# Performance work log

Hardware: AMD Instinct MI355X
Metric: run time of the kernel (lower is better)

Reference implementation:

```python
import jax, jax.numpy as jnp
import numpy as np

N = 100000      # nodes
E = 1600000     # edges (avg degree 16)
DIN = 128
DOUT = 128


def setup_inputs() -> dict:
    key = jax.random.key(0)
    k1, k2, k3, k4 = jax.random.split(key, 4)
    x = jax.random.normal(k1, (N, DIN), dtype=jnp.float32)
    edge_index = jax.random.randint(k2, (2, E), 0, N, dtype=jnp.int64)
    # guarantee every node appears at least once as a source row so that
    # degree > 0 everywhere (1/sqrt(0) would be inf, as in the torch code)
    row = edge_index[0].at[:N].set(jnp.arange(N, dtype=jnp.int64))
    edge_index = jnp.stack([row, edge_index[1]])
    W = jax.random.normal(k3, (DOUT, DIN), dtype=jnp.float32) / np.sqrt(DIN)
    b = jax.random.normal(k4, (DOUT,), dtype=jnp.float32) * 0.01
    return {"x": x, "edge_index": edge_index, "W": W, "b": b}


def reference(x, edge_index, W, b):
    # Math identical to: A = dense(add_self_loops(edge_index));
    # D = 1/sqrt(degree(edge_index[0]))  (degree WITHOUT self-loops);
    # out = (D_i * A_ij * D_j) @ (x W^T + b)
    row, col = edge_index[0], edge_index[1]
    deg = jax.ops.segment_sum(jnp.ones(row.shape[0], x.dtype), row, num_segments=N)
    d = jax.lax.rsqrt(deg)                      # [N]
    h = x @ W.T + b                             # [N, DOUT]
    # edge contributions: out[r] += D[r] * D[c] * h[c]  (duplicate edges sum, as to_dense does)
    agg = jax.ops.segment_sum(d[col][:, None] * h[col], row, num_segments=N)
    # self-loop term added for every node: D[i]^2 * h[i]
    out = d[:, None] * agg + (d * d)[:, None] * h
    return out
```

## Files before the change

### kernel.cpp

```cpp
#include <hip/hip_runtime.h>

#define D 128
#define BROWS 512
#define LOGB 9
#define NBMAX 256
#define CAP 9216
#define CHUNK 4096

typedef __attribute__((ext_vector_type(8))) short bf16x8;
typedef __attribute__((ext_vector_type(4))) float f32x4;

__device__ inline unsigned short f2bf(float f) {
    unsigned u = __float_as_uint(f);
    u += 0x7FFFu + ((u >> 16) & 1u);
    return (unsigned short)(u >> 16);
}
__device__ inline float bf2f(unsigned short h) {
    return __uint_as_float((unsigned)h << 16);
}
__device__ inline float bflo(unsigned u) { return __uint_as_float(u << 16); }
__device__ inline float bfhi(unsigned u) { return __uint_as_float(u & 0xFFFF0000u); }

__global__ __launch_bounds__(512) void k_bin(const int* __restrict__ row,
                                             const int* __restrict__ col,
                                             int E, int* __restrict__ gcur,
                                             unsigned* __restrict__ ebuf,
                                             const float* __restrict__ W,
                                             unsigned short* __restrict__ Wbh,
                                             unsigned short* __restrict__ Wbl) {
    __shared__ int lhist[NBMAX];
    __shared__ int sc[NBMAX];
    __shared__ int gbase[NBMAX];
    __shared__ unsigned sstage[CHUNK];
    __shared__ int sdest[CHUNK];
    int t = threadIdx.x;
    if (blockIdx.x < 8) {
        int base = blockIdx.x * 2048 + t;
        #pragma unroll
        for (int i = 0; i < 4; ++i) {
            int idx = base + i * 512;
            float wv = W[idx];
            unsigned short h = f2bf(wv);
            Wbh[idx] = h;
            Wbl[idx] = f2bf(wv - bf2f(h));
        }
    }
    int base = blockIdx.x * CHUNK;
    if (t < NBMAX) lhist[t] = 0;
    __syncthreads();
    int b[8], p[8]; unsigned pk[8];
    #pragma unroll
    for (int i = 0; i < 8; ++i) {
        int idx = base + i * 512 + t;
        if (idx < E) {
            int r = row[idx], c = col[idx];
            b[i] = r >> LOGB;
            pk[i] = ((unsigned)(r & (BROWS - 1)) << 17) | (unsigned)c;
            p[i] = atomicAdd(&lhist[b[i]], 1);
        } else b[i] = -1;
    }
    __syncthreads();
    if (t < 64) {
        int a0 = lhist[4*t], a1 = lhist[4*t+1], a2 = lhist[4*t+2], a3 = lhist[4*t+3];
        int s = a0 + a1 + a2 + a3;
        int incl = s;
        #pragma unroll
        for (int m = 1; m < 64; m <<= 1) {
            int tmp = __shfl_up(incl, m);
            if (t >= m) incl += tmp;
        }
        int excl = incl - s;
        sc[4*t] = excl; sc[4*t+1] = excl + a0;
        sc[4*t+2] = excl + a0 + a1; sc[4*t+3] = excl + a0 + a1 + a2;
        if (a0 > 0) gbase[4*t]   = atomicAdd(&gcur[4*t],   a0);
        if (a1 > 0) gbase[4*t+1] = atomicAdd(&gcur[4*t+1], a1);
        if (a2 > 0) gbase[4*t+2] = atomicAdd(&gcur[4*t+2], a2);
        if (a3 > 0) gbase[4*t+3] = atomicAdd(&gcur[4*t+3], a3);
    }
    __syncthreads();
    #pragma unroll
    for (int i = 0; i < 8; ++i) {
        if (b[i] >= 0) {
            int lidx = sc[b[i]] + p[i];
            int rel = gbase[b[i]] + p[i];
            sstage[lidx] = pk[i];
            sdest[lidx] = (rel < CAP) ? (b[i] * CAP + rel) : -1;
        }
    }
    __syncthreads();
    int total = sc[NBMAX - 1] + lhist[NBMAX - 1];
    for (int i = t; i < total; i += 512) {
        int d = sdest[i];
        if (d >= 0) ebuf[d] = sstage[i];
    }
}

__global__ __launch_bounds__(1024) void k_group(const int* __restrict__ gcur,
                                                const unsigned* __restrict__ ebuf,
                                                const float* __restrict__ x,
                                                int N, int NBK,
                                                float* __restrict__ dvals,
                                                int* __restrict__ rptr,
                                                int* __restrict__ csr_col,
                                                unsigned short* __restrict__ xs) {
    __shared__ unsigned sebuf[CAP];
    __shared__ int lhist[BROWS];
    __shared__ float sdl[BROWS];
    __shared__ int wtot[8];
    __shared__ int woff[8];
    __shared__ int sebase;
    int bkt = blockIdx.x, t = threadIdx.x;
    int cnt = gcur[bkt]; if (cnt > CAP) cnt = CAP;
    if (t < 64) {
        int acc = 0;
        for (int i = t; i < bkt; i += 64) {
            int g = gcur[i];
            acc += (g > CAP) ? CAP : g;
        }
        #pragma unroll
        for (int m = 1; m < 64; m <<= 1) acc += __shfl_xor(acc, m);
        if (t == 0) sebase = acc;
    }
    if (t < BROWS) lhist[t] = 0;
    __syncthreads();
    const unsigned* ep = ebuf + (size_t)bkt * CAP;
    for (int i = t; i < cnt; i += 1024) {
        unsigned e = ep[i];
        sebuf[i] = e;
        atomicAdd(&lhist[e >> 17], 1);
    }
    __syncthreads();
    int lane = t & 63, wv = t >> 6;
    int v = 0, incl = 0;
    if (t < BROWS) {
        v = lhist[t];
        incl = v;
        #pragma unroll
        for (int m = 1; m < 64; m <<= 1) {
            int tmp = __shfl_up(incl, m);
            if (lane >= m) incl += tmp;
        }
        if (lane == 63) wtot[wv] = incl;
    }
    __syncthreads();
    if (t < 8) {
        int w = wtot[t];
        int wincl = w;
        #pragma unroll
        for (int m = 1; m < 8; m <<= 1) {
            int tmp = __shfl_up(wincl, m);
            if (t >= m) wincl += tmp;
        }
        woff[t] = wincl - w;
    }
    __syncthreads();
    int ebase = sebase;
    if (t < BROWS) {
        int excl = woff[wv] + incl - v;
        int r = (bkt << LOGB) + t;
        float dl = rsqrtf((float)v);
        if (r < N) {
            rptr[r] = ebase + excl;
            dvals[r] = dl;
        }
        sdl[t] = dl;
        lhist[t] = excl;
    }
    if (bkt == NBK - 1 && t == 0) rptr[N] = ebase + cnt;
    if (bkt == 0 && t == 0) dvals[N] = 0.f;
    __syncthreads();
    for (int i = t; i < cnt; i += 1024) {
        unsigned e = sebuf[i];
        int rr = (int)(e >> 17);
        int p = atomicAdd(&lhist[rr], 1);
        csr_col[ebase + p] = (int)(e & 0x1FFFFu);
    }
    int rb = bkt << LOGB;
    const float4* x4 = (const float4*)x;
    for (int idx = t; idx < BROWS * 32; idx += 1024) {
        int rl = idx >> 5;
        int r = rb + rl;
        if (r < N) {
            float4 vv = x4[(size_t)r * 32 + (idx & 31)];
            float d = sdl[rl];
            ushort4 o = make_ushort4(f2bf(d * vv.x), f2bf(d * vv.y),
                                     f2bf(d * vv.z), f2bf(d * vv.w));
            ((ushort4*)xs)[(size_t)r * 32 + (idx & 31)] = o;
        }
    }
    if (bkt == 0 && t < 64)
        ((unsigned*)(xs + (size_t)N * D))[t] = 0u;
}

#define ACC8(v) do { \
    a[0] += bflo((v).x); a[1] += bfhi((v).x); \
    a[2] += bflo((v).y); a[3] += bfhi((v).y); \
    a[4] += bflo((v).z); a[5] += bfhi((v).z); \
    a[6] += bflo((v).w); a[7] += bfhi((v).w); } while (0)

__global__ __launch_bounds__(256) void k_rows(const unsigned short* __restrict__ xs,
                                              const int* __restrict__ rptr,
                                              const int* __restrict__ csr_col,
                                              const float* __restrict__ dvals,
                                              float* __restrict__ ssum,
                                              float* __restrict__ y, int N) {
    int wid = (blockIdx.x * blockDim.x + threadIdx.x) >> 6;
    if (wid >= N) return;
    int lane = threadIdx.x & 63;
    int grp = lane >> 4, sl = lane & 15;
    int s = rptr[wid];
    int n = rptr[wid + 1] - s;
    const uint4* xsv = (const uint4*)xs;

    int cc = csr_col[s + lane];
    int ccreg = (lane < n) ? cc : N;
    float sd = dvals[ccreg];
    uint4 vself = xsv[(size_t)wid * 16 + sl];

    float a[8] = {0.f, 0.f, 0.f, 0.f, 0.f, 0.f, 0.f, 0.f};
    int nf = (n < 64) ? n : 64;
    for (int k0 = 0; k0 < nf; k0 += 16) {
        int i0 = k0 + grp;
        int c0 = __shfl(ccreg, i0);
        int c1 = __shfl(ccreg, i0 + 4);
        int c2 = __shfl(ccreg, i0 + 8);
        int c3 = __shfl(ccreg, i0 + 12);
        uint4 v0 = xsv[(size_t)c0 * 16 + sl];
        uint4 v1 = xsv[(size_t)c1 * 16 + sl];
        uint4 v2 = xsv[(size_t)c2 * 16 + sl];
        uint4 v3 = xsv[(size_t)c3 * 16 + sl];
        __builtin_amdgcn_sched_group_barrier(0x020, 4, 0);
        ACC8(v0); ACC8(v1); ACC8(v2); ACC8(v3);
        __builtin_amdgcn_sched_group_barrier(0x002, 64, 0);
    }
    if (__builtin_expect(n > 64, 0)) {
        for (int idx = 64 + grp; idx < n; idx += 4) {
            int c = csr_col[s + idx];
            uint4 v = xsv[(size_t)c * 16 + sl];
            ACC8(v);
        }
        for (int idx = 64 + lane; idx < n; idx += 64)
            sd += dvals[csr_col[s + idx]];
    }
    if (grp == 0) ACC8(vself);

    #pragma unroll
    for (int j = 0; j < 8; ++j) {
        a[j] += __shfl_xor(a[j], 16);
        a[j] += __shfl_xor(a[j], 32);
    }
    #pragma unroll
    for (int m = 1; m < 64; m <<= 1) sd += __shfl_xor(sd, m);

    float dr = dvals[wid];
    if (grp < 2) {
        float4 o = (grp == 0) ? make_float4(a[0], a[1], a[2], a[3])
                              : make_float4(a[4], a[5], a[6], a[7]);
        o.x *= dr; o.y *= dr; o.z *= dr; o.w *= dr;
        ((float4*)(y + (size_t)wid * D))[sl * 2 + grp] = o;
    }
    if (lane == 0) ssum[wid] = dr * (dr + sd);
}

#define LDSW 136

__global__ __launch_bounds__(256, 2) void k_gemm(const unsigned short* __restrict__ Wbh,
                                                 const unsigned short* __restrict__ Wbl,
                                                 const float* __restrict__ b,
                                                 const float* __restrict__ ssum,
                                                 float* yo, int N) {
    __shared__ unsigned short Whi[128 * LDSW];
    __shared__ unsigned short Wlo[128 * LDSW];
    __shared__ float bs[D];
    int t = threadIdx.x;
    #pragma unroll
    for (int i = 0; i < 16; ++i) {
        int idx4 = i * 256 + t;
        int r = idx4 >> 5;
        int c = (idx4 & 31) * 4;
        ((ushort4*)&Whi[r * LDSW + c])[0] = ((const ushort4*)Wbh)[idx4];
        ((ushort4*)&Wlo[r * LDSW + c])[0] = ((const ushort4*)Wbl)[idx4];
    }
    if (t < D) bs[t] = b[t];
    __syncthreads();

    int wave = t >> 6, lane = t & 63;
    int quad = lane >> 4, mrow = lane & 15;
    int row_base = blockIdx.x * 128 + wave * 32;

    bf16x8 Ahi[2][4], Alo[2][4];
    #pragma unroll
    for (int s = 0; s < 2; ++s) {
        int grow = row_base + s * 16 + mrow;
        bool ok = grow < N;
        const float* yrow = yo + (size_t)(ok ? grow : 0) * D;
        #pragma unroll
        for (int kk = 0; kk < 4; ++kk) {
            int k0 = kk * 32 + quad * 8;
            float4 f0 = ok ? ((const float4*)(yrow + k0))[0] : make_float4(0, 0, 0, 0);
            float4 f1 = ok ? ((const float4*)(yrow + k0))[1] : make_float4(0, 0, 0, 0);
            float fv[8] = {f0.x, f0.y, f0.z, f0.w, f1.x, f1.y, f1.z, f1.w};
            #pragma unroll
            for (int j = 0; j < 8; ++j) {
                unsigned short h = f2bf(fv[j]);
                Ahi[s][kk][j] = (short)h;
                Alo[s][kk][j] = (short)f2bf(fv[j] - bf2f(h));
            }
        }
    }

    f32x4 acc[2][8];
    #pragma unroll
    for (int s = 0; s < 2; ++s)
        #pragma unroll
        for (int ct = 0; ct < 8; ++ct)
            acc[s][ct] = (f32x4){0.f, 0.f, 0.f, 0.f};

    #pragma unroll
    for (int ct = 0; ct < 8; ++ct) {
        int wrow = ct * 16 + mrow;
        #pragma unroll
        for (int kk = 0; kk < 4; ++kk) {
            int off = wrow * LDSW + kk * 32 + quad * 8;
            bf16x8 Bhi = *(const bf16x8*)&Whi[off];
            bf16x8 Blo = *(const bf16x8*)&Wlo[off];
            #pragma unroll
            for (int s = 0; s < 2; ++s) {
                acc[s][ct] = __builtin_amdgcn_mfma_f32_16x16x32_bf16(Ahi[s][kk], Bhi, acc[s][ct], 0, 0, 0);
                acc[s][ct] = __builtin_amdgcn_mfma_f32_16x16x32_bf16(Alo[s][kk], Bhi, acc[s][ct], 0, 0, 0);
                acc[s][ct] = __builtin_amdgcn_mfma_f32_16x16x32_bf16(Ahi[s][kk], Blo, acc[s][ct], 0, 0, 0);
            }
        }
    }

    #pragma unroll
    for (int s = 0; s < 2; ++s) {
        #pragma unroll
        for (int r = 0; r < 4; ++r) {
            int grow = row_base + s * 16 + quad * 4 + r;
            if (grow < N) {
                float sv = ssum[grow];
                #pragma unroll
                for (int ct = 0; ct < 8; ++ct) {
                    int col = ct * 16 + mrow;
                    yo[(size_t)grow * D + col] = acc[s][ct][r] + sv * bs[col];
                }
            }
        }
    }
}

extern "C" void kernel_launch(void* const* d_in, const int* in_sizes, int n_in,
                              void* d_out, int out_size, void* d_ws, size_t ws_size,
                              hipStream_t stream) {
    const float* x  = (const float*)d_in[0];
    const int*   ei = (const int*)d_in[1];
    const float* W  = (const float*)d_in[2];
    const float* b  = (const float*)d_in[3];
    float* out = (float*)d_out;
    int N = in_sizes[0] / D;
    int E = in_sizes[1] / 2;
    int NB = (N + BROWS - 1) / BROWS;
    int NCH = (E + CHUNK - 1) / CHUNK;

    int*            gcur    = (int*)d_ws;
    int*            rptr    = gcur + NBMAX;
    float*          dvals   = (float*)(rptr + N + 1);
    float*          ssum    = dvals + N + 1;
    int*            csr_col = (int*)(ssum + N);
    unsigned*       ebuf    = (unsigned*)(csr_col + E + 64);
    unsigned short* Wbh     = (unsigned short*)(ebuf + (size_t)NB * CAP);
    unsigned short* Wbl     = Wbh + D * D;
    uintptr_t xs_addr = (uintptr_t)(Wbl + D * D);
    xs_addr = (xs_addr + 15) & ~(uintptr_t)15;
    unsigned short* xs = (unsigned short*)xs_addr;

    hipMemsetAsync(gcur, 0, NBMAX * sizeof(int), stream);
    k_bin<<<NCH, 512, 0, stream>>>(ei, ei + E, E, gcur, ebuf, W, Wbh, Wbl);
    k_group<<<NB, 1024, 0, stream>>>(gcur, ebuf, x, N, NB, dvals, rptr, csr_col, xs);
    k_rows<<<(N + 3) / 4, 256, 0, stream>>>(xs, rptr, csr_col, dvals, ssum, out, N);
    k_gemm<<<(N + 127) / 128, 256, 0, stream>>>(Wbh, Wbl, b, ssum, out, N);
}
```

Baseline: 275.3 us.

## Reorder pipeline: transform first, then aggregate pre-scaled bf16 H

```diff
diff --git a/kernel.cpp b/kernel.cpp
--- a/kernel.cpp
+++ b/kernel.cpp
@@ -6,6 +6,7 @@
 #define NBMAX 256
 #define CAP 9216
 #define CHUNK 4096
+#define LDSW 136
 
 typedef __attribute__((ext_vector_type(8))) short bf16x8;
 typedef __attribute__((ext_vector_type(4))) float f32x4;
@@ -97,15 +98,13 @@
 
 __global__ __launch_bounds__(1024) void k_group(const int* __restrict__ gcur,
                                                 const unsigned* __restrict__ ebuf,
-                                                const float* __restrict__ x,
                                                 int N, int NBK,
                                                 float* __restrict__ dvals,
                                                 int* __restrict__ rptr,
                                                 int* __restrict__ csr_col,
-                                                unsigned short* __restrict__ xs) {
+                                                unsigned short* __restrict__ Hs) {
     __shared__ unsigned sebuf[CAP];
     __shared__ int lhist[BROWS];
-    __shared__ float sdl[BROWS];
     __shared__ int wtot[8];
     __shared__ int woff[8];
     __shared__ int sebase;
@@ -158,16 +157,16 @@
     if (t < BROWS) {
         int excl = woff[wv] + incl - v;
         int r = (bkt << LOGB) + t;
-        float dl = rsqrtf((float)v);
         if (r < N) {
             rptr[r] = ebase + excl;
-            dvals[r] = dl;
-        }
-        sdl[t] = dl;
+            dvals[r] = rsqrtf((float)v);
+        }
         lhist[t] = excl;
     }
     if (bkt == NBK - 1 && t == 0) rptr[N] = ebase + cnt;
     if (bkt == 0 && t == 0) dvals[N] = 0.f;
+    if (bkt == 0 && t < 64)
+        ((unsigned*)(Hs + (size_t)N * D))[t] = 0u;
     __syncthreads();
     for (int i = t; i < cnt; i += 1024) {
         unsigned e = sebuf[i];
@@ -175,100 +174,14 @@
         int p = atomicAdd(&lhist[rr], 1);
         csr_col[ebase + p] = (int)(e & 0x1FFFFu);
     }
-    int rb = bkt << LOGB;
-    const float4* x4 = (const float4*)x;
-    for (int idx = t; idx < BROWS * 32; idx += 1024) {
-        int rl = idx >> 5;
-        int r = rb + rl;
-        if (r < N) {
-            float4 vv = x4[(size_t)r * 32 + (idx & 31)];
-            float d = sdl[rl];
-            ushort4 o = make_ushort4(f2bf(d * vv.x), f2bf(d * vv.y),
-                                     f2bf(d * vv.z), f2bf(d * vv.w));
-            ((ushort4*)xs)[(size_t)r * 32 + (idx & 31)] = o;
-        }
-    }
-    if (bkt == 0 && t < 64)
-        ((unsigned*)(xs + (size_t)N * D))[t] = 0u;
-}
-
-#define ACC8(v) do { \
-    a[0] += bflo((v).x); a[1] += bfhi((v).x); \
-    a[2] += bflo((v).y); a[3] += bfhi((v).y); \
-    a[4] += bflo((v).z); a[5] += bfhi((v).z); \
-    a[6] += bflo((v).w); a[7] += bfhi((v).w); } while (0)
-
-__global__ __launch_bounds__(256) void k_rows(const unsigned short* __restrict__ xs,
-                                              const int* __restrict__ rptr,
-                                              const int* __restrict__ csr_col,
-                                              const float* __restrict__ dvals,
-                                              float* __restrict__ ssum,
-                                              float* __restrict__ y, int N) {
-    int wid = (blockIdx.x * blockDim.x + threadIdx.x) >> 6;
-    if (wid >= N) return;
-    int lane = threadIdx.x & 63;
-    int grp = lane >> 4, sl = lane & 15;
-    int s = rptr[wid];
-    int n = rptr[wid + 1] - s;
-    const uint4* xsv = (const uint4*)xs;
-
-    int cc = csr_col[s + lane];
-    int ccreg = (lane < n) ? cc : N;
-    float sd = dvals[ccreg];
-    uint4 vself = xsv[(size_t)wid * 16 + sl];
-
-    float a[8] = {0.f, 0.f, 0.f, 0.f, 0.f, 0.f, 0.f, 0.f};
-    int nf = (n < 64) ? n : 64;
-    for (int k0 = 0; k0 < nf; k0 += 16) {
-        int i0 = k0 + grp;
-        int c0 = __shfl(ccreg, i0);
-        int c1 = __shfl(ccreg, i0 + 4);
-        int c2 = __shfl(ccreg, i0 + 8);
-        int c3 = __shfl(ccreg, i0 + 12);
-        uint4 v0 = xsv[(size_t)c0 * 16 + sl];
-        uint4 v1 = xsv[(size_t)c1 * 16 + sl];
-        uint4 v2 = xsv[(size_t)c2 * 16 + sl];
-        uint4 v3 = xsv[(size_t)c3 * 16 + sl];
-        __builtin_amdgcn_sched_group_barrier(0x020, 4, 0);
-        ACC8(v0); ACC8(v1); ACC8(v2); ACC8(v3);
-        __builtin_amdgcn_sched_group_barrier(0x002, 64, 0);
-    }
-    if (__builtin_expect(n > 64, 0)) {
-        for (int idx = 64 + grp; idx < n; idx += 4) {
-            int c = csr_col[s + idx];
-            uint4 v = xsv[(size_t)c * 16 + sl];
-            ACC8(v);
-        }
-        for (int idx = 64 + lane; idx < n; idx += 64)
-            sd += dvals[csr_col[s + idx]];
-    }
-    if (grp == 0) ACC8(vself);
-
-    #pragma unroll
-    for (int j = 0; j < 8; ++j) {
-        a[j] += __shfl_xor(a[j], 16);
-        a[j] += __shfl_xor(a[j], 32);
-    }
-    #pragma unroll
-    for (int m = 1; m < 64; m <<= 1) sd += __shfl_xor(sd, m);
-
-    float dr = dvals[wid];
-    if (grp < 2) {
-        float4 o = (grp == 0) ? make_float4(a[0], a[1], a[2], a[3])
-                              : make_float4(a[4], a[5], a[6], a[7]);
-        o.x *= dr; o.y *= dr; o.z *= dr; o.w *= dr;
-        ((float4*)(y + (size_t)wid * D))[sl * 2 + grp] = o;
-    }
-    if (lane == 0) ssum[wid] = dr * (dr + sd);
-}
-
-#define LDSW 136
-
-__global__ __launch_bounds__(256, 2) void k_gemm(const unsigned short* __restrict__ Wbh,
-                                                 const unsigned short* __restrict__ Wbl,
-                                                 const float* __restrict__ b,
-                                                 const float* __restrict__ ssum,
-                                                 float* yo, int N) {
+}
+
+__global__ __launch_bounds__(256, 2) void k_gc(const float* __restrict__ x,
+                                               const unsigned short* __restrict__ Wbh,
+                                               const unsigned short* __restrict__ Wbl,
+                                               const float* __restrict__ b,
+                                               const float* __restrict__ dvals,
+                                               unsigned short* __restrict__ Hs, int N) {
     __shared__ unsigned short Whi[128 * LDSW];
     __shared__ unsigned short Wlo[128 * LDSW];
     __shared__ float bs[D];
@@ -293,12 +206,12 @@
     for (int s = 0; s < 2; ++s) {
         int grow = row_base + s * 16 + mrow;
         bool ok = grow < N;
-        const float* yrow = yo + (size_t)(ok ? grow : 0) * D;
+        const float* xrow = x + (size_t)(ok ? grow : 0) * D;
         #pragma unroll
         for (int kk = 0; kk < 4; ++kk) {
             int k0 = kk * 32 + quad * 8;
-            float4 f0 = ok ? ((const float4*)(yrow + k0))[0] : make_float4(0, 0, 0, 0);
-            float4 f1 = ok ? ((const float4*)(yrow + k0))[1] : make_float4(0, 0, 0, 0);
+            float4 f0 = ok ? ((const float4*)(xrow + k0))[0] : make_float4(0, 0, 0, 0);
+            float4 f1 = ok ? ((const float4*)(xrow + k0))[1] : make_float4(0, 0, 0, 0);
             float fv[8] = {f0.x, f0.y, f0.z, f0.w, f1.x, f1.y, f1.z, f1.w};
             #pragma unroll
             for (int j = 0; j < 8; ++j) {
@@ -333,20 +246,90 @@
         }
     }
 
+    __syncthreads();
+    unsigned short* stage = Whi;
     #pragma unroll
     for (int s = 0; s < 2; ++s) {
         #pragma unroll
         for (int r = 0; r < 4; ++r) {
             int grow = row_base + s * 16 + quad * 4 + r;
-            if (grow < N) {
-                float sv = ssum[grow];
-                #pragma unroll
-                for (int ct = 0; ct < 8; ++ct) {
-                    int col = ct * 16 + mrow;
-                    yo[(size_t)grow * D + col] = acc[s][ct][r] + sv * bs[col];
-                }
+            float dv = dvals[(grow < N) ? grow : N];
+            int lrow = wave * 32 + s * 16 + quad * 4 + r;
+            #pragma unroll
+            for (int ct = 0; ct < 8; ++ct) {
+                int col = ct * 16 + mrow;
+                stage[lrow * LDSW + col] = f2bf(dv * (acc[s][ct][r] + bs[col]));
             }
         }
+    }
+    __syncthreads();
+    for (int i = t; i < 128 * 16; i += 256) {
+        int lrow = i >> 4;
+        int g = i & 15;
+        int grow = blockIdx.x * 128 + lrow;
+        if (grow < N)
+            ((uint4*)Hs)[(size_t)grow * 16 + g] =
+                ((const uint4*)&stage[lrow * LDSW])[g];
+    }
+}
+
+#define ACC8(v) do { \
+    a[0] += bflo((v).x); a[1] += bfhi((v).x); \
+    a[2] += bflo((v).y); a[3] += bfhi((v).y); \
+    a[4] += bflo((v).z); a[5] += bfhi((v).z); \
+    a[6] += bflo((v).w); a[7] += bfhi((v).w); } while (0)
+
+__global__ __launch_bounds__(256) void k_rows(const unsigned short* __restrict__ Hs,
+                                              const int* __restrict__ rptr,
+                                              const int* __restrict__ csr_col,
+                                              const float* __restrict__ dvals,
+                                              float* __restrict__ out, int N) {
+    int wid = (blockIdx.x * blockDim.x + threadIdx.x) >> 6;
+    if (wid >= N) return;
+    int lane = threadIdx.x & 63;
+    int grp = lane >> 4, sl = lane & 15;
+    int s = rptr[wid];
+    int n = rptr[wid + 1] - s;
+    const uint4* hv = (const uint4*)Hs;
+
+    int cc = csr_col[s + lane];
+    int ccreg = (lane < n) ? cc : N;
+    uint4 vself = hv[(size_t)wid * 16 + sl];
+
+    float a[8] = {0.f, 0.f, 0.f, 0.f, 0.f, 0.f, 0.f, 0.f};
+    int nf = (n < 64) ? n : 64;
+    for (int k0 = 0; k0 < nf; k0 += 16) {
+        int i0 = k0 + grp;
+        int c0 = __shfl(ccreg, i0);
+        int c1 = __shfl(ccreg, i0 + 4);
+        int c2 = __shfl(ccreg, i0 + 8);
+        int c3 = __shfl(ccreg, i0 + 12);
+        uint4 v0 = hv[(size_t)c0 * 16 + sl];
+        uint4 v1 = hv[(size_t)c1 * 16 + sl];
+        uint4 v2 = hv[(size_t)c2 * 16 + sl];
+        uint4 v3 = hv[(size_t)c3 * 16 + sl];
+        ACC8(v0); ACC8(v1); ACC8(v2); ACC8(v3);
+    }
+    if (__builtin_expect(n > 64, 0)) {
+        for (int idx = 64 + grp; idx < n; idx += 4) {
+            int c = csr_col[s + idx];
+            uint4 v = hv[(size_t)c * 16 + sl];
+            ACC8(v);
+        }
+    }
+    if (grp == 0) ACC8(vself);
+
+    #pragma unroll
+    for (int j = 0; j < 8; ++j) {
+        a[j] += __shfl_xor(a[j], 16);
+        a[j] += __shfl_xor(a[j], 32);
+    }
+    float dr = dvals[wid];
+    if (grp < 2) {
+        float4 o = (grp == 0) ? make_float4(a[0], a[1], a[2], a[3])
+                              : make_float4(a[4], a[5], a[6], a[7]);
+        o.x *= dr; o.y *= dr; o.z *= dr; o.w *= dr;
+        ((float4*)(out + (size_t)wid * D))[sl * 2 + grp] = o;
     }
 }
 
@@ -366,18 +349,17 @@
     int*            gcur    = (int*)d_ws;
     int*            rptr    = gcur + NBMAX;
     float*          dvals   = (float*)(rptr + N + 1);
-    float*          ssum    = dvals + N + 1;
-    int*            csr_col = (int*)(ssum + N);
+    int*            csr_col = (int*)(dvals + N + 1);
     unsigned*       ebuf    = (unsigned*)(csr_col + E + 64);
     unsigned short* Wbh     = (unsigned short*)(ebuf + (size_t)NB * CAP);
     unsigned short* Wbl     = Wbh + D * D;
-    uintptr_t xs_addr = (uintptr_t)(Wbl + D * D);
-    xs_addr = (xs_addr + 15) & ~(uintptr_t)15;
-    unsigned short* xs = (unsigned short*)xs_addr;
+    uintptr_t hs_addr = (uintptr_t)(Wbl + D * D);
+    hs_addr = (hs_addr + 15) & ~(uintptr_t)15;
+    unsigned short* Hs = (unsigned short*)hs_addr;
 
     hipMemsetAsync(gcur, 0, NBMAX * sizeof(int), stream);
     k_bin<<<NCH, 512, 0, stream>>>(ei, ei + E, E, gcur, ebuf, W, Wbh, Wbl);
-    k_group<<<NB, 1024, 0, stream>>>(gcur, ebuf, x, N, NB, dvals, rptr, csr_col, xs);
-    k_rows<<<(N + 3) / 4, 256, 0, stream>>>(xs, rptr, csr_col, dvals, ssum, out, N);
-    k_gemm<<<(N + 127) / 128, 256, 0, stream>>>(Wbh, Wbl, b, ssum, out, N);
-}
+    k_group<<<NB, 1024, 0, stream>>>(gcur, ebuf, N, NB, dvals, rptr, csr_col, Hs);
+    k_gc<<<(N + 127) / 128, 256, 0, stream>>>(x, Wbh, Wbl, b, dvals, Hs, N);
+    k_rows<<<(N + 3) / 4, 256, 0, stream>>>(Hs, rptr, csr_col, dvals, out, N);
+}
```

New measurement: 248.9 us. 1.11x faster.
